# Performance work log

Hardware: AMD Instinct MI355X
Metric: run time of the kernel (lower is better)

Reference implementation:

```python
import jax, jax.numpy as jnp
import numpy as np

B, C, H, W = 4, 64, 64, 64
C8 = C // 8


def cl_attention(x, gamma):
    # DANet CAM-style channel attention: [B,C,H,W] -> [B,C,H,W]
    b, c, h, w = x.shape
    xf = x.reshape(b, c, h * w)                       # b c n
    energy = jnp.einsum('bcn,bdn->bcd', xf, xf)       # b c c
    energy = jnp.max(energy, axis=-1, keepdims=True) - energy
    attn = jax.nn.softmax(energy, axis=-1)
    out = jnp.einsum('bcd,bdn->bcn', attn, xf).reshape(b, c, h, w)
    return gamma * out + x


def setup_inputs() -> dict:
    key = jax.random.key(0)
    ks = jax.random.split(key, 8)
    s = 0.02
    return {
        'cnn_feat': jax.random.normal(ks[0], (B, C, H, W), jnp.float32),
        'vit_feat': jax.random.normal(ks[1], (B, C, H, W), jnp.float32),
        'Wq': jax.random.normal(ks[2], (C8, C), jnp.float32) * s,   # 1x1 conv kernel
        'bq': jnp.zeros((C8,), jnp.float32),
        'Wk': jax.random.normal(ks[3], (C8, C), jnp.float32) * s,
        'bk': jnp.zeros((C8,), jnp.float32),
        'Wv': jax.random.normal(ks[4], (C, C), jnp.float32) * s,
        'bv': jnp.zeros((C,), jnp.float32),
        'gamma': jnp.zeros((1,), jnp.float32),
        'gamma_cla_cnn': jnp.zeros((1,), jnp.float32),
        'gamma_cla_vit': jnp.zeros((1,), jnp.float32),
    }


def reference(cnn_feat, vit_feat, Wq, bq, Wk, bk, Wv, bv, gamma,
              gamma_cla_cnn, gamma_cla_vit):
    b, c, h, w = cnn_feat.shape
    n = h * w

    cnn_att = cl_attention(cnn_feat, gamma_cla_cnn)   # b c h w
    vit_att = cl_attention(vit_feat, gamma_cla_vit)   # b c h w

    # query: 1x1 conv -> view(b, C8, n) -> permute -> (b, n, C8)
    q = jnp.einsum('bchw,oc->bhwo', cnn_att, Wq).reshape(b, n, -1) + bq

    # vit: rearrange 'b c h w -> b (h w) c'
    vit_flat = vit_att.reshape(b, c, n).transpose(0, 2, 1)          # b n c
    k = vit_flat @ Wk.T + bk                                        # b n C8
    v = vit_flat @ Wv.T + bv                                        # b n C

    energy = jnp.einsum('bqd,bkd->bqk', q, k)                       # b n n
    attn = jax.nn.softmax(energy, axis=-1)
    out = jnp.einsum('bqk,bkc->bqc', attn, v)                       # b n c
    out = out.transpose(0, 2, 1).reshape(b, c, h, w)                # 'b (h w) c -> b c h w'
    return gamma * out + cnn_feat
```

## Files before the change

kernel.cpp:

```cpp
#include <hip/hip_runtime.h>
#include <hip/hip_bf16.h>

#define BSZ 4
#define CC 64
#define NN 4096
#define CN (CC*NN)
#define BCN (BSZ*CN)

typedef __attribute__((ext_vector_type(4))) float    f4v;
typedef __attribute__((ext_vector_type(4))) int      i4v;
typedef __attribute__((ext_vector_type(2))) unsigned u2v;
typedef __attribute__((ext_vector_type(8))) short    s8v;

#define DPP_F(x_, ctrl_) __builtin_bit_cast(float, \
    __builtin_amdgcn_update_dpp(0, __builtin_bit_cast(int, (float)(x_)), (ctrl_), 0xf, 0xf, true))
#define QP_X1 0xB1

__device__ __forceinline__ unsigned pack_bf16(float lo, float hi) {
    unsigned l = __builtin_bit_cast(unsigned, lo);
    unsigned h = __builtin_bit_cast(unsigned, hi);
    return (h & 0xFFFF0000u) | (l >> 16);
}

__global__ __launch_bounds__(256) void gram_k(const float* __restrict__ cnn,
                                              const float* __restrict__ vit,
                                              float* __restrict__ part) {
    __shared__ __align__(16) float sXT[64*68];
    int t = threadIdx.x;
    int blk = blockIdx.x;
    int ch = blk & 63, b = (blk >> 6) & 3, i2 = blk >> 8;
    const float* X = (i2 ? vit : cnn) + b * CN;
    int n0 = ch * 64;
#pragma unroll
    for (int j = 0; j < 4; j++) {
        int idx = t + j * 256;
        int c = idx >> 4, n4 = idx & 15;
        f4v val = *(const f4v*)&X[c * NN + n0 + n4 * 4];
        int base = (n4 * 4) * 68 + c;
        sXT[base]       = val[0];
        sXT[base + 68]  = val[1];
        sXT[base + 136] = val[2];
        sXT[base + 204] = val[3];
    }
    __syncthreads();
    int tc = (t & 15) * 4, td = (t >> 4) * 4;
    f4v acc[4];
#pragma unroll
    for (int i = 0; i < 4; i++) acc[i] = (f4v){0.f, 0.f, 0.f, 0.f};
    for (int k = 0; k < 64; k++) {
        f4v a  = *(const f4v*)&sXT[k * 68 + tc];
        f4v bb = *(const f4v*)&sXT[k * 68 + td];
#pragma unroll
        for (int i = 0; i < 4; i++) acc[i] += a[i] * bb;
    }
    float* dst = part + ch * 32768 + (i2 * 4 + b) * 4096;
#pragma unroll
    for (int i = 0; i < 4; i++) *(f4v*)&dst[(tc + i) * 64 + td] = acc[i];
}

__global__ void gred_k(const float* __restrict__ part, float* __restrict__ G) {
    int row = blockIdx.x;
    int d = threadIdx.x;
    float s = 0.f;
#pragma unroll 8
    for (int ch = 0; ch < 64; ch++) s += part[ch * 32768 + row * 64 + d];
    float mn = s;
#pragma unroll
    for (int off = 1; off < 64; off <<= 1) mn = fminf(mn, __shfl_xor(mn, off));
    float e = __expf(mn - s);
    float sm = e;
#pragma unroll
    for (int off = 1; off < 64; off <<= 1) sm += __shfl_xor(sm, off);
    G[row * 64 + d] = e / sm;
}

__global__ __launch_bounds__(256) void weff_k(const float* __restrict__ G,
                                              const float* __restrict__ Wq,
                                              const float* __restrict__ Wk,
                                              const float* __restrict__ Wv,
                                              const float* __restrict__ gcnn,
                                              const float* __restrict__ gvit,
                                              ushort* __restrict__ WeffB) {
    __shared__ float sA[8192];
    __shared__ float sWt[1024];
    int t = threadIdx.x;
    int b = blockIdx.x / 5, tile = blockIdx.x % 5;
    for (int i = t; i < 4096; i += 256) {
        sA[i]        = G[b * 4096 + i];
        sA[4096 + i] = G[(4 + b) * 4096 + i];
    }
    __syncthreads();
    float gc = *gcnn, gv = *gvit;
#pragma unroll
    for (int k = 0; k < 4; k++) {
        int idx = k * 256 + t;
        int r = idx >> 6, c = idx & 63;
        const float* Wrow; const float* A; float g;
        if (tile == 0) {
            if (r < 8) { Wrow = Wq + r * 64;       A = sA;        g = gc; }
            else       { Wrow = Wk + (r - 8) * 64; A = sA + 4096; g = gv; }
        } else         { Wrow = Wv + ((tile - 1) * 16 + r) * 64; A = sA + 4096; g = gv; }
        float s = 0.f;
#pragma unroll 8
        for (int d = 0; d < 64; d++) s += Wrow[d] * A[d * 64 + c];
        sWt[idx] = g * s + Wrow[c];
    }
    __syncthreads();
    if (t < 128) {
        int frag = t >> 6, lane = t & 63, m = lane & 15, q4 = lane >> 4;
        i4v o;
#pragma unroll
        for (int p = 0; p < 4; p++) {
            int c0 = frag * 32 + q4 * 8 + 2 * p;
            o[p] = (int)pack_bf16(sWt[m * 64 + c0], sWt[m * 64 + c0 + 1]);
        }
        *(i4v*)&WeffB[(size_t)(b * 10 + tile * 2 + frag) * 512 + lane * 8] = o;
    }
}

__global__ __launch_bounds__(256) void qkv_k(const float* __restrict__ cnn,
                                             const float* __restrict__ vit,
                                             const ushort* __restrict__ WeffB,
                                             const float* __restrict__ bq,
                                             const float* __restrict__ bk,
                                             const float* __restrict__ bv,
                                             ushort* __restrict__ qb, ushort* __restrict__ kb,
                                             ushort* __restrict__ vT) {
    int t = threadIdx.x;
    int b = blockIdx.x >> 6, n0 = (blockIdx.x & 63) * 64;
    int w = t >> 6, lane = t & 63, c15 = lane & 15, q4 = lane >> 4;
    int n = n0 + w * 16 + c15;
    const float LOG2E = 1.44269504f;

    s8v A[10];
    const ushort* WB = WeffB + (size_t)b * 5120 + lane * 8;
#pragma unroll
    for (int i = 0; i < 10; i++)
        A[i] = __builtin_bit_cast(s8v, *(const i4v*)(WB + (size_t)i * 512));

    s8v Bc[2], Bv[2];
#pragma unroll
    for (int f = 0; f < 2; f++) {
        i4v pc, pv;
#pragma unroll
        for (int p = 0; p < 4; p++) {
            int c0 = f * 32 + q4 * 8 + p * 2;
            size_t a0 = (size_t)b * CN + (size_t)c0 * NN + n;
            pc[p] = (int)pack_bf16(cnn[a0], cnn[a0 + NN]);
            pv[p] = (int)pack_bf16(vit[a0], vit[a0 + NN]);
        }
        Bc[f] = __builtin_bit_cast(s8v, pc);
        Bv[f] = __builtin_bit_cast(s8v, pv);
    }

    f4v acc = *(const f4v*)(bq + (q4 & 1) * 4);
    acc = __builtin_amdgcn_mfma_f32_16x16x32_bf16(A[0], Bc[0], acc, 0, 0, 0);
    acc = __builtin_amdgcn_mfma_f32_16x16x32_bf16(A[1], Bc[1], acc, 0, 0, 0);
    if (q4 < 2) {
        unsigned d0 = pack_bf16(acc[0] * LOG2E, acc[1] * LOG2E);
        unsigned d1 = pack_bf16(acc[2] * LOG2E, acc[3] * LOG2E);
        unsigned long long v = ((unsigned long long)d1 << 32) | d0;
        *(unsigned long long*)&qb[(size_t)(b * NN + n) * 8 + q4 * 4] = v;
    }
    acc = *(const f4v*)(bk + (q4 & 1) * 4);
    acc = __builtin_amdgcn_mfma_f32_16x16x32_bf16(A[0], Bv[0], acc, 0, 0, 0);
    acc = __builtin_amdgcn_mfma_f32_16x16x32_bf16(A[1], Bv[1], acc, 0, 0, 0);
    if (q4 >= 2) {
        unsigned d0 = pack_bf16(acc[0], acc[1]), d1 = pack_bf16(acc[2], acc[3]);
        unsigned long long v = ((unsigned long long)d1 << 32) | d0;
        *(unsigned long long*)&kb[(size_t)(b * NN + n) * 8 + (q4 - 2) * 4] = v;
    }
#pragma unroll
    for (int tile = 1; tile < 5; tile++) {
        acc = *(const f4v*)(bv + (tile - 1) * 16 + q4 * 4);
        acc = __builtin_amdgcn_mfma_f32_16x16x32_bf16(A[tile * 2],     Bv[0], acc, 0, 0, 0);
        acc = __builtin_amdgcn_mfma_f32_16x16x32_bf16(A[tile * 2 + 1], Bv[1], acc, 0, 0, 0);
#pragma unroll
        for (int r = 0; r < 4; r++) {
            float other = DPP_F(acc[r], QP_X1);
            unsigned pkd = (lane & 1) ? pack_bf16(other, acc[r])
                                      : pack_bf16(acc[r], other);
            if (!(lane & 1)) {
                int row = (tile - 1) * 16 + q4 * 4 + r;
                *(unsigned*)&vT[(size_t)(b * 64 + row) * NN + n] = pkd;
            }
        }
    }
}

__global__ __launch_bounds__(256, 2) void flash_k(const ushort* __restrict__ qb,
                                                  const ushort* __restrict__ kb,
                                                  const ushort* __restrict__ vT,
                                                  float* __restrict__ pOT,
                                                  float* __restrict__ pm,
                                                  float* __restrict__ pl) {
    __shared__ __align__(16) unsigned P[4608];
    int t = threadIdx.x;
    int lane = t & 63, w = t >> 6;
    int c15 = lane & 15, q4 = lane >> 4;
    int blk = blockIdx.x;
    int s = blk >> 7, b = (blk >> 5) & 3, q0 = (blk & 31) * 128;
    unsigned* Pw = P + w * 1152;

    s8v qB[2];
#pragma unroll
    for (int g = 0; g < 2; g++) {
        i4v qa = (i4v){0, 0, 0, 0};
        if (q4 == 0)
            qa = *(const i4v*)(qb + (size_t)(b * NN + q0 + w * 32 + g * 16 + c15) * 8);
        qB[g] = __builtin_bit_cast(s8v, qa);
    }
    i4v onesi; onesi[0] = onesi[1] = onesi[2] = onesi[3] = 0x3F803F80;
    s8v ones = __builtin_bit_cast(s8v, onesi);

    f4v accO[2][4];
#pragma unroll
    for (int g = 0; g < 2; g++)
#pragma unroll
        for (int nt = 0; nt < 4; nt++) accO[g][nt] = (f4v){0.f, 0.f, 0.f, 0.f};
    f4v accl[2] = {(f4v){0.f,0.f,0.f,0.f}, (f4v){0.f,0.f,0.f,0.f}};
    float m_[2] = {-1e30f, -1e30f};

    const ushort* kbb = kb + (size_t)b * NN * 8;
    const ushort* vbase = vT + (size_t)b * 64 * NN + (size_t)c15 * NN + q4 * 8;

    int kt0 = s * 16;
    i4v bkf[4];
#pragma unroll
    for (int nt = 0; nt < 4; nt++)
        bkf[nt] = *(const i4v*)(kbb + (size_t)(kt0 * 64 + nt * 16 + c15) * 8);

    for (int kt = kt0; kt < kt0 + 16; kt++) {
        int k0 = kt * 64;
        i4v vb0[4], vb1[4];
#pragma unroll
        for (int nt = 0; nt < 4; nt++) {
            const ushort* vp = vbase + (size_t)nt * 16 * NN + k0;
            vb0[nt] = *(const i4v*)vp;
            vb1[nt] = *(const i4v*)(vp + 32);
        }

        f4v z = (f4v){0.f, 0.f, 0.f, 0.f};
        f4v S[2][4];
#pragma unroll
        for (int g = 0; g < 2; g++)
#pragma unroll
            for (int nt = 0; nt < 4; nt++)
                S[g][nt] = __builtin_amdgcn_mfma_f32_16x16x32_bf16(
                    __builtin_bit_cast(s8v, bkf[nt]), qB[g], z, 0, 0, 0);

        int ktn = (kt + 1 < kt0 + 16) ? kt + 1 : kt;
        i4v nbkf[4];
#pragma unroll
        for (int nt = 0; nt < 4; nt++)
            nbkf[nt] = *(const i4v*)(kbb + (size_t)(ktn * 64 + nt * 16 + c15) * 8);

        float al[2];
#pragma unroll
        for (int g = 0; g < 2; g++) {
            f4v m4 = __builtin_elementwise_max(
                __builtin_elementwise_max(S[g][0], S[g][1]),
                __builtin_elementwise_max(S[g][2], S[g][3]));
            float mx = fmaxf(fmaxf(m4[0], m4[1]), fmaxf(m4[2], m4[3]));
            mx = fmaxf(mx, __shfl_xor(mx, 16));
            mx = fmaxf(mx, __shfl_xor(mx, 32));
            float mnew = fmaxf(m_[g], mx);
            al[g] = __builtin_amdgcn_exp2f(m_[g] - mnew);
            m_[g] = mnew;
            unsigned* Pg = Pw + g * 576 + c15 * 36;
#pragma unroll
            for (int nt = 0; nt < 4; nt++) {
                float p0 = __builtin_amdgcn_exp2f(S[g][nt][0] - mnew);
                float p1 = __builtin_amdgcn_exp2f(S[g][nt][1] - mnew);
                float p2 = __builtin_amdgcn_exp2f(S[g][nt][2] - mnew);
                float p3 = __builtin_amdgcn_exp2f(S[g][nt][3] - mnew);
                u2v d2; d2[0] = pack_bf16(p0, p1); d2[1] = pack_bf16(p2, p3);
                *(u2v*)&Pg[nt * 8 + 2 * q4] = d2;
            }
#pragma unroll
            for (int nt = 0; nt < 4; nt++) accO[g][nt] *= al[g];
            accl[g] *= al[g];
        }

#pragma unroll
        for (int g = 0; g < 2; g++) {
            i4v pb0 = *(i4v*)&Pw[g * 576 + c15 * 36 + 4 * q4];
            i4v pb1 = *(i4v*)&Pw[g * 576 + c15 * 36 + 16 + 4 * q4];
            s8v B0 = __builtin_bit_cast(s8v, pb0);
            s8v B1 = __builtin_bit_cast(s8v, pb1);
            accl[g] = __builtin_amdgcn_mfma_f32_16x16x32_bf16(ones, B0, accl[g], 0, 0, 0);
            accl[g] = __builtin_amdgcn_mfma_f32_16x16x32_bf16(ones, B1, accl[g], 0, 0, 0);
#pragma unroll
            for (int nt = 0; nt < 4; nt++) {
                accO[g][nt] = __builtin_amdgcn_mfma_f32_16x16x32_bf16(
                    __builtin_bit_cast(s8v, vb0[nt]), B0, accO[g][nt], 0, 0, 0);
                accO[g][nt] = __builtin_amdgcn_mfma_f32_16x16x32_bf16(
                    __builtin_bit_cast(s8v, vb1[nt]), B1, accO[g][nt], 0, 0, 0);
            }
        }
#pragma unroll
        for (int nt = 0; nt < 4; nt++) bkf[nt] = nbkf[nt];
    }

#pragma unroll
    for (int g = 0; g < 2; g++) {
        int qg = q0 + w * 32 + g * 16 + c15;
#pragma unroll
        for (int nt = 0; nt < 4; nt++)
#pragma unroll
            for (int r = 0; r < 4; r++) {
                int c = nt * 16 + q4 * 4 + r;
                pOT[(size_t)((s * 4 + b) * 64 + c) * NN + qg] = accO[g][nt][r];
            }
        if (q4 == 0) {
            pm[(size_t)(s * 4 + b) * NN + qg] = m_[g];
            pl[(size_t)(s * 4 + b) * NN + qg] = accl[g][0];
        }
    }
}

__global__ __launch_bounds__(256) void comb_k(const float* __restrict__ pOT,
                                              const float* __restrict__ pm,
                                              const float* __restrict__ pl,
                                              const float* __restrict__ cnn,
                                              const float* __restrict__ gamma,
                                              float* __restrict__ out) {
    int t = threadIdx.x;
    int b = blockIdx.x >> 6, n0 = (blockIdx.x & 63) * 64;
    int nq = t & 15, cl = t >> 4;
    int n = n0 + nq * 4;
    f4v pmv[4], plv[4];
#pragma unroll
    for (int s = 0; s < 4; s++) {
        pmv[s] = *(const f4v*)&pm[(size_t)(s * 4 + b) * NN + n];
        plv[s] = *(const f4v*)&pl[(size_t)(s * 4 + b) * NN + n];
    }
    f4v M = __builtin_elementwise_max(__builtin_elementwise_max(pmv[0], pmv[1]),
                                      __builtin_elementwise_max(pmv[2], pmv[3]));
    f4v wsc[4], L = (f4v){0.f, 0.f, 0.f, 0.f};
#pragma unroll
    for (int s = 0; s < 4; s++) {
        f4v e;
#pragma unroll
        for (int j = 0; j < 4; j++) e[j] = __builtin_amdgcn_exp2f(pmv[s][j] - M[j]);
        wsc[s] = e;
        L += e * plv[s];
    }
    float g = *gamma;
    f4v rv;
#pragma unroll
    for (int j = 0; j < 4; j++) rv[j] = g / L[j];
#pragma unroll
    for (int it = 0; it < 4; it++) {
        int c = it * 16 + cl;
        f4v o = (f4v){0.f, 0.f, 0.f, 0.f};
#pragma unroll
        for (int s = 0; s < 4; s++)
            o += wsc[s] * *(const f4v*)&pOT[(size_t)((s * 4 + b) * 64 + c) * NN + n];
        size_t gi = (size_t)(b * 64 + c) * NN + n;
        f4v cv = *(const f4v*)&cnn[gi];
        *(f4v*)&out[gi] = o * rv + cv;
    }
}

extern "C" void kernel_launch(void* const* d_in, const int* in_sizes, int n_in,
                              void* d_out, int out_size, void* d_ws, size_t ws_size,
                              hipStream_t stream) {
    const float* cnn  = (const float*)d_in[0];
    const float* vit  = (const float*)d_in[1];
    const float* Wq   = (const float*)d_in[2];
    const float* bq   = (const float*)d_in[3];
    const float* Wk   = (const float*)d_in[4];
    const float* bk   = (const float*)d_in[5];
    const float* Wv   = (const float*)d_in[6];
    const float* bv   = (const float*)d_in[7];
    const float* gam  = (const float*)d_in[8];
    const float* gcnn = (const float*)d_in[9];
    const float* gvit = (const float*)d_in[10];
    float* out = (float*)d_out;

    float* ws = (float*)d_ws;
    float*  pOT   = ws;
    float*  part  = ws;
    float*  G     = ws + 4194304;
    ushort* WeffB = (ushort*)(ws + 4227072);
    ushort* qb    = (ushort*)(ws + 4237312);
    ushort* kb    = (ushort*)(ws + 4302848);
    ushort* vT    = (ushort*)(ws + 4368384);
    float*  pm    = ws + 4892672;
    float*  pl    = ws + 4958208;

    gram_k <<<512, 256, 0, stream>>>(cnn, vit, part);
    gred_k <<<512, 64,  0, stream>>>(part, G);
    weff_k <<<20,  256, 0, stream>>>(G, Wq, Wk, Wv, gcnn, gvit, WeffB);
    qkv_k  <<<256, 256, 0, stream>>>(cnn, vit, WeffB, bq, bk, bv, qb, kb, vT);
    flash_k<<<512, 256, 0, stream>>>(qb, kb, vT, pOT, pm, pl);
    comb_k <<<256, 256, 0, stream>>>(pOT, pm, pl, cnn, gam, out);
}
```

Before: 147.0 us.

## Keep softmax probabilities in registers and double key splits in flash kernel

The flash kernel no longer stages P through shared memory. The exp'd scores are packed straight into MFMA B operands, and V is loaded with a permuted layout so that the accumulator layout matches. The row sum is now a scalar register accumulation plus a final shuffle, replacing the ones-MFMA. The key dimension is split 8 ways instead of 4, giving 1024 blocks, with launch bounds raised to 4 blocks per SM and the workspace and combine kernel resized to match. This is meant to remove LDS round trips and raise occupancy and parallelism, at the cost of more partial output traffic in the combine kernel and no K prefetch.

Result: slower. 188.2 us (+28.0%).

```diff
diff --git a/kernel.cpp b/kernel.cpp
--- a/kernel.cpp
+++ b/kernel.cpp
@@ -9,6 +9,7 @@
 
 typedef __attribute__((ext_vector_type(4))) float    f4v;
 typedef __attribute__((ext_vector_type(4))) int      i4v;
+typedef __attribute__((ext_vector_type(2))) int      i2v;
 typedef __attribute__((ext_vector_type(2))) unsigned u2v;
 typedef __attribute__((ext_vector_type(8))) short    s8v;
 
@@ -188,19 +189,17 @@
     }
 }
 
-__global__ __launch_bounds__(256, 2) void flash_k(const ushort* __restrict__ qb,
+__global__ __launch_bounds__(256, 4) void flash_k(const ushort* __restrict__ qb,
                                                   const ushort* __restrict__ kb,
                                                   const ushort* __restrict__ vT,
                                                   float* __restrict__ pOT,
                                                   float* __restrict__ pm,
                                                   float* __restrict__ pl) {
-    __shared__ __align__(16) unsigned P[4608];
     int t = threadIdx.x;
     int lane = t & 63, w = t >> 6;
     int c15 = lane & 15, q4 = lane >> 4;
     int blk = blockIdx.x;
     int s = blk >> 7, b = (blk >> 5) & 3, q0 = (blk & 31) * 128;
-    unsigned* Pw = P + w * 1152;
 
     s8v qB[2];
 #pragma unroll
@@ -210,35 +209,27 @@
             qa = *(const i4v*)(qb + (size_t)(b * NN + q0 + w * 32 + g * 16 + c15) * 8);
         qB[g] = __builtin_bit_cast(s8v, qa);
     }
-    i4v onesi; onesi[0] = onesi[1] = onesi[2] = onesi[3] = 0x3F803F80;
-    s8v ones = __builtin_bit_cast(s8v, onesi);
 
     f4v accO[2][4];
 #pragma unroll
     for (int g = 0; g < 2; g++)
 #pragma unroll
         for (int nt = 0; nt < 4; nt++) accO[g][nt] = (f4v){0.f, 0.f, 0.f, 0.f};
-    f4v accl[2] = {(f4v){0.f,0.f,0.f,0.f}, (f4v){0.f,0.f,0.f,0.f}};
+    float lacc[2] = {0.f, 0.f};
     float m_[2] = {-1e30f, -1e30f};
 
-    const ushort* kbb = kb + (size_t)b * NN * 8;
-    const ushort* vbase = vT + (size_t)b * 64 * NN + (size_t)c15 * NN + q4 * 8;
-
-    int kt0 = s * 16;
-    i4v bkf[4];
+    const ushort* kbb = kb + (size_t)b * NN * 8 + (size_t)c15 * 8;
+    const ushort* vrow[4];
 #pragma unroll
     for (int nt = 0; nt < 4; nt++)
-        bkf[nt] = *(const i4v*)(kbb + (size_t)(kt0 * 64 + nt * 16 + c15) * 8);
-
-    for (int kt = kt0; kt < kt0 + 16; kt++) {
-        int k0 = kt * 64;
-        i4v vb0[4], vb1[4];
-#pragma unroll
-        for (int nt = 0; nt < 4; nt++) {
-            const ushort* vp = vbase + (size_t)nt * 16 * NN + k0;
-            vb0[nt] = *(const i4v*)vp;
-            vb1[nt] = *(const i4v*)(vp + 32);
-        }
+        vrow[nt] = vT + (size_t)(b * 64 + nt * 16 + c15) * NN + 4 * q4;
+
+    for (int kt = 0; kt < 8; kt++) {
+        int k0 = (s * 8 + kt) * 64;
+        i4v bkf[4];
+#pragma unroll
+        for (int nt = 0; nt < 4; nt++)
+            bkf[nt] = *(const i4v*)(kbb + (size_t)(k0 + nt * 16) * 8);
 
         f4v z = (f4v){0.f, 0.f, 0.f, 0.f};
         f4v S[2][4];
@@ -249,13 +240,17 @@
                 S[g][nt] = __builtin_amdgcn_mfma_f32_16x16x32_bf16(
                     __builtin_bit_cast(s8v, bkf[nt]), qB[g], z, 0, 0, 0);
 
-        int ktn = (kt + 1 < kt0 + 16) ? kt + 1 : kt;
-        i4v nbkf[4];
-#pragma unroll
-        for (int nt = 0; nt < 4; nt++)
-            nbkf[nt] = *(const i4v*)(kbb + (size_t)(ktn * 64 + nt * 16 + c15) * 8);
-
-        float al[2];
+        i4v vA[2][4];
+#pragma unroll
+        for (int F = 0; F < 2; F++)
+#pragma unroll
+            for (int nt = 0; nt < 4; nt++) {
+                i2v x = *(const i2v*)(vrow[nt] + k0 + 32 * F);
+                i2v y = *(const i2v*)(vrow[nt] + k0 + 32 * F + 16);
+                vA[F][nt] = (i4v){x[0], x[1], y[0], y[1]};
+            }
+
+        s8v Bp[2][2];
 #pragma unroll
         for (int g = 0; g < 2; g++) {
             f4v m4 = __builtin_elementwise_max(
@@ -265,41 +260,47 @@
             mx = fmaxf(mx, __shfl_xor(mx, 16));
             mx = fmaxf(mx, __shfl_xor(mx, 32));
             float mnew = fmaxf(m_[g], mx);
-            al[g] = __builtin_amdgcn_exp2f(m_[g] - mnew);
+            float al = __builtin_amdgcn_exp2f(m_[g] - mnew);
             m_[g] = mnew;
-            unsigned* Pg = Pw + g * 576 + c15 * 36;
+            float ps = 0.f;
+            f4v p[4];
 #pragma unroll
             for (int nt = 0; nt < 4; nt++) {
-                float p0 = __builtin_amdgcn_exp2f(S[g][nt][0] - mnew);
-                float p1 = __builtin_amdgcn_exp2f(S[g][nt][1] - mnew);
-                float p2 = __builtin_amdgcn_exp2f(S[g][nt][2] - mnew);
-                float p3 = __builtin_amdgcn_exp2f(S[g][nt][3] - mnew);
-                u2v d2; d2[0] = pack_bf16(p0, p1); d2[1] = pack_bf16(p2, p3);
-                *(u2v*)&Pg[nt * 8 + 2 * q4] = d2;
-            }
-#pragma unroll
-            for (int nt = 0; nt < 4; nt++) accO[g][nt] *= al[g];
-            accl[g] *= al[g];
-        }
-
-#pragma unroll
-        for (int g = 0; g < 2; g++) {
-            i4v pb0 = *(i4v*)&Pw[g * 576 + c15 * 36 + 4 * q4];
-            i4v pb1 = *(i4v*)&Pw[g * 576 + c15 * 36 + 16 + 4 * q4];
-            s8v B0 = __builtin_bit_cast(s8v, pb0);
-            s8v B1 = __builtin_bit_cast(s8v, pb1);
-            accl[g] = __builtin_amdgcn_mfma_f32_16x16x32_bf16(ones, B0, accl[g], 0, 0, 0);
-            accl[g] = __builtin_amdgcn_mfma_f32_16x16x32_bf16(ones, B1, accl[g], 0, 0, 0);
-#pragma unroll
-            for (int nt = 0; nt < 4; nt++) {
-                accO[g][nt] = __builtin_amdgcn_mfma_f32_16x16x32_bf16(
-                    __builtin_bit_cast(s8v, vb0[nt]), B0, accO[g][nt], 0, 0, 0);
-                accO[g][nt] = __builtin_amdgcn_mfma_f32_16x16x32_bf16(
-                    __builtin_bit_cast(s8v, vb1[nt]), B1, accO[g][nt], 0, 0, 0);
-            }
-        }
-#pragma unroll
-        for (int nt = 0; nt < 4; nt++) bkf[nt] = nbkf[nt];
+#pragma unroll
+                for (int r = 0; r < 4; r++) {
+                    p[nt][r] = __builtin_amdgcn_exp2f(S[g][nt][r] - mnew);
+                    ps += p[nt][r];
+                }
+            }
+#pragma unroll
+            for (int F = 0; F < 2; F++) {
+                i4v bp;
+                bp[0] = (int)pack_bf16(p[2 * F][0],     p[2 * F][1]);
+                bp[1] = (int)pack_bf16(p[2 * F][2],     p[2 * F][3]);
+                bp[2] = (int)pack_bf16(p[2 * F + 1][0], p[2 * F + 1][1]);
+                bp[3] = (int)pack_bf16(p[2 * F + 1][2], p[2 * F + 1][3]);
+                Bp[g][F] = __builtin_bit_cast(s8v, bp);
+            }
+            lacc[g] = lacc[g] * al + ps;
+#pragma unroll
+            for (int nt = 0; nt < 4; nt++) accO[g][nt] *= al;
+        }
+
+#pragma unroll
+        for (int F = 0; F < 2; F++)
+#pragma unroll
+            for (int g = 0; g < 2; g++)
+#pragma unroll
+                for (int nt = 0; nt < 4; nt++)
+                    accO[g][nt] = __builtin_amdgcn_mfma_f32_16x16x32_bf16(
+                        __builtin_bit_cast(s8v, vA[F][nt]), Bp[g][F],
+                        accO[g][nt], 0, 0, 0);
+    }
+
+#pragma unroll
+    for (int g = 0; g < 2; g++) {
+        lacc[g] += __shfl_xor(lacc[g], 16);
+        lacc[g] += __shfl_xor(lacc[g], 32);
     }
 
 #pragma unroll
@@ -314,7 +315,7 @@
             }
         if (q4 == 0) {
             pm[(size_t)(s * 4 + b) * NN + qg] = m_[g];
-            pl[(size_t)(s * 4 + b) * NN + qg] = accl[g][0];
+            pl[(size_t)(s * 4 + b) * NN + qg] = lacc[g];
         }
     }
 }
@@ -329,22 +330,21 @@
     int b = blockIdx.x >> 6, n0 = (blockIdx.x & 63) * 64;
     int nq = t & 15, cl = t >> 4;
     int n = n0 + nq * 4;
-    f4v pmv[4], plv[4];
-#pragma unroll
-    for (int s = 0; s < 4; s++) {
+    f4v pmv[8];
+    f4v M = (f4v){-1e30f, -1e30f, -1e30f, -1e30f};
+#pragma unroll
+    for (int s = 0; s < 8; s++) {
         pmv[s] = *(const f4v*)&pm[(size_t)(s * 4 + b) * NN + n];
-        plv[s] = *(const f4v*)&pl[(size_t)(s * 4 + b) * NN + n];
-    }
-    f4v M = __builtin_elementwise_max(__builtin_elementwise_max(pmv[0], pmv[1]),
-                                      __builtin_elementwise_max(pmv[2], pmv[3]));
-    f4v wsc[4], L = (f4v){0.f, 0.f, 0.f, 0.f};
-#pragma unroll
-    for (int s = 0; s < 4; s++) {
+        M = __builtin_elementwise_max(M, pmv[s]);
+    }
+    f4v wsc[8], L = (f4v){0.f, 0.f, 0.f, 0.f};
+#pragma unroll
+    for (int s = 0; s < 8; s++) {
         f4v e;
 #pragma unroll
         for (int j = 0; j < 4; j++) e[j] = __builtin_amdgcn_exp2f(pmv[s][j] - M[j]);
         wsc[s] = e;
-        L += e * plv[s];
+        L += e * *(const f4v*)&pl[(size_t)(s * 4 + b) * NN + n];
     }
     float g = *gamma;
     f4v rv;
@@ -355,7 +355,7 @@
         int c = it * 16 + cl;
         f4v o = (f4v){0.f, 0.f, 0.f, 0.f};
 #pragma unroll
-        for (int s = 0; s < 4; s++)
+        for (int s = 0; s < 8; s++)
             o += wsc[s] * *(const f4v*)&pOT[(size_t)((s * 4 + b) * 64 + c) * NN + n];
         size_t gi = (size_t)(b * 64 + c) * NN + n;
         f4v cv = *(const f4v*)&cnn[gi];
@@ -382,18 +382,18 @@
     float* ws = (float*)d_ws;
     float*  pOT   = ws;
     float*  part  = ws;
-    float*  G     = ws + 4194304;
-    ushort* WeffB = (ushort*)(ws + 4227072);
-    ushort* qb    = (ushort*)(ws + 4237312);
-    ushort* kb    = (ushort*)(ws + 4302848);
-    ushort* vT    = (ushort*)(ws + 4368384);
-    float*  pm    = ws + 4892672;
-    float*  pl    = ws + 4958208;
-
-    gram_k <<<512, 256, 0, stream>>>(cnn, vit, part);
-    gred_k <<<512, 64,  0, stream>>>(part, G);
-    weff_k <<<20,  256, 0, stream>>>(G, Wq, Wk, Wv, gcnn, gvit, WeffB);
-    qkv_k  <<<256, 256, 0, stream>>>(cnn, vit, WeffB, bq, bk, bv, qb, kb, vT);
-    flash_k<<<512, 256, 0, stream>>>(qb, kb, vT, pOT, pm, pl);
-    comb_k <<<256, 256, 0, stream>>>(pOT, pm, pl, cnn, gam, out);
-}
+    float*  G     = ws + 8388608;
+    ushort* WeffB = (ushort*)(ws + 8421376);
+    ushort* qb    = (ushort*)(ws + 8431616);
+    ushort* kb    = (ushort*)(ws + 8497152);
+    ushort* vT    = (ushort*)(ws + 8562688);
+    float*  pm    = ws + 9086976;
+    float*  pl    = ws + 9218048;
+
+    gram_k <<<512,  256, 0, stream>>>(cnn, vit, part);
+    gred_k <<<512,  64,  0, stream>>>(part, G);
+    weff_k <<<20,   256, 0, stream>>>(G, Wq, Wk, Wv, gcnn, gvit, WeffB);
+    qkv_k  <<<256,  256, 0, stream>>>(cnn, vit, WeffB, bq, bk, bv, qb, kb, vT);
+    flash_k<<<1024, 256, 0, stream>>>(qb, kb, vT, pOT, pm, pl);
+    comb_k <<<256,  256, 0, stream>>>(pOT, pm, pl, cnn, gam, out);
+}
```
